# Kernel tuning notes

Hardware: AMD Instinct MI355X
Metric: run time of the kernel (lower is better)

Reference implementation:

```python
import jax, jax.numpy as jnp
import numpy as np

# Block sizes: 3-hop sampled bipartite graphs (src -> dst per layer)
N_SRC0, N_DST0, E0 = 500_000, 100_000, 1_000_000
N_DST1, E1 = 10_000, 100_000
N_DST2, E2 = 1_024, 10_240
D_IN, D_HID, N_CLS = 128, 128, 47


def setup_inputs() -> dict:
    key = jax.random.key(0)
    ks = jax.random.split(key, 16)
    feats = jax.random.normal(ks[0], (N_SRC0, D_IN), dtype=jnp.float32)
    src0 = jax.random.randint(ks[1], (E0,), 0, N_SRC0)
    dst0 = jax.random.randint(ks[2], (E0,), 0, N_DST0)
    src1 = jax.random.randint(ks[3], (E1,), 0, N_DST0)
    dst1 = jax.random.randint(ks[4], (E1,), 0, N_DST1)
    src2 = jax.random.randint(ks[5], (E2,), 0, N_DST1)
    dst2 = jax.random.randint(ks[6], (E2,), 0, N_DST2)
    # fsi.inverse_idx reindex + NPFeatureShuffle all-to-all -> two permutations
    inverse_idx = jax.random.permutation(ks[7], N_DST0)
    shuffle_idx = jax.random.permutation(ks[8], N_DST0)
    def glorot(k, fan_in, fan_out):
        lim = np.sqrt(6.0 / (fan_in + fan_out)).astype(np.float32)
        return jax.random.uniform(k, (fan_in, fan_out), jnp.float32, -lim, lim)
    W0 = glorot(ks[9], D_IN, D_HID)
    b0 = jnp.zeros((D_HID,), jnp.float32)
    W1 = glorot(ks[10], D_HID, D_HID)
    b1 = jnp.zeros((D_HID,), jnp.float32)
    W2 = glorot(ks[11], D_HID, N_CLS)
    b2 = jnp.zeros((N_CLS,), jnp.float32)
    return dict(feats=feats, src0=src0, dst0=dst0, src1=src1, dst1=dst1,
                src2=src2, dst2=dst2, inverse_idx=inverse_idx,
                shuffle_idx=shuffle_idx, W0=W0, b0=b0, W1=W1, b1=b1, W2=W2, b2=b2)


def _graph_conv(h_src, src, dst, n_src, n_dst, W, b, norm_both):
    # DGL GraphConv: optional D^{-1/2} on src, W, sum-aggregate over edges,
    # optional D^{-1/2} on dst, + bias. Degrees clamped to min 1.
    ones = jnp.ones(src.shape[0], dtype=h_src.dtype)
    if norm_both:
        out_deg = jax.ops.segment_sum(ones, src, num_segments=n_src)
        h_src = h_src * jax.lax.rsqrt(jnp.clip(out_deg, 1.0, None))[:, None]
    msgs = (h_src @ W)[src]                      # [E, d_out] gather
    agg = jax.ops.segment_sum(msgs, dst, num_segments=n_dst)  # scatter-add
    if norm_both:
        in_deg = jax.ops.segment_sum(ones, dst, num_segments=n_dst)
        agg = agg * jax.lax.rsqrt(jnp.clip(in_deg, 1.0, None))[:, None]
    return agg + b


def reference(feats, src0, dst0, src1, dst1, src2, dst2,
              inverse_idx, shuffle_idx, W0, b0, W1, b1, W2, b2):
    # layer 0: norm='none'
    h = _graph_conv(feats, src0, dst0, N_SRC0, N_DST0, W0, b0, norm_both=False)
    # fsi.inverse_idx reindex + NPFeatureShuffle (modeled as permutations)
    h = h[inverse_idx]
    h = h[shuffle_idx]
    h = jax.nn.relu(h)  # dropout is identity in eval
    # layer 1: norm='both'
    h = _graph_conv(h, src1, dst1, N_DST0, N_DST1, W1, b1, norm_both=True)
    h = jax.nn.relu(h)
    # layer 2: norm='both'
    h = _graph_conv(h, src2, dst2, N_DST1, N_DST2, W2, b2, norm_both=True)
    return h
```

## Files before the change

kernel.cpp:

```cpp
#include <hip/hip_runtime.h>
#include <stdint.h>

typedef unsigned int u32;
typedef unsigned short u16;

#define N_SRC0 500000
#define N_DST0 100000
#define N_DST1 10000
#define N_DST2 1024
#define NCLS 47
#define GROWS 48

#define NB0 98
#define NB1 10
#define NB2 1
#define NBLK 109

static __device__ __forceinline__ float bf16_lo(u32 v) { return __uint_as_float(v << 16); }
static __device__ __forceinline__ float bf16_hi(u32 v) { return __uint_as_float(v & 0xffff0000u); }
static __device__ __forceinline__ float bf16_to_f(u16 s) { return __uint_as_float(((u32)s) << 16); }
static __device__ __forceinline__ u16 f_to_bf16(float f) {
    u32 u = __float_as_uint(f);
    u32 r = u + 0x7fffu + ((u >> 16) & 1u);
    return (u16)(r >> 16);
}

#define OFF_A      0u
#define OFF_T1     0u
#define OFF_X2     6000000u
#define OFF_T2     12000000u
#define OFF_X1     51200000u
#define OFF_CSR0   102400000u
#define OFF_CSR1   106400000u
#define OFF_CSR2   106800000u
#define OFF_RS0    106840960u
#define OFF_CUR0   107240976u
#define OFF_RS1    107640976u
#define OFF_CUR1   107680992u
#define OFF_RS2    107720992u
#define OFF_CUR2   107725104u
#define OFF_CNT0   107729200u
#define OFF_DS1    108129200u
#define OFF_DD1    108529200u
#define OFF_DS2    108569200u
#define OFF_DD2    108609200u
#define ZERO_OFF   OFF_CNT0
#define ZERO_BYTES 884096u
#define OFF_WC0    108613296u
#define OFF_BC0    108678832u
#define OFF_WC1    108679344u
#define OFF_BC1    108744880u
#define OFF_WC2    108745392u
#define OFF_BC2    108769456u
#define OFF_FLAG   108769712u
#define OFF_BSUM   108769776u
#define OFF_BOFF   108770224u

__global__ __launch_bounds__(256) void k_zero(float4* __restrict__ p, int n) {
    int i = blockIdx.x * 256 + threadIdx.x;
    int stride = gridDim.x * 256;
    float4 z = make_float4(0.f, 0.f, 0.f, 0.f);
    for (; i < n; i += stride) p[i] = z;
}

__global__ void k_detect(const u32* __restrict__ w, u32* __restrict__ flag) {
    u32 u = w[threadIdx.x];
    int e = (u >> 23) & 0xff;
    unsigned long long m = __ballot(e >= 0xC0);
    if (threadIdx.x == 0) *flag = (m != 0ull) ? 1u : 0u;
}

__global__ __launch_bounds__(256) void k_convw(
    const void* __restrict__ W0, const void* __restrict__ b0,
    const void* __restrict__ W1, const void* __restrict__ b1,
    const void* __restrict__ W2, const void* __restrict__ b2,
    float* __restrict__ Wc0, float* __restrict__ bc0,
    float* __restrict__ Wc1, float* __restrict__ bc1,
    float* __restrict__ Wc2, float* __restrict__ bc2,
    const u32* __restrict__ flag)
{
    int i = blockIdx.x * 256 + threadIdx.x;
    bool bf = (*flag != 0u);
    const void* src; float* dst; int j;
    if      (i < 16384) { src = W0; dst = Wc0; j = i; }
    else if (i < 16512) { src = b0; dst = bc0; j = i - 16384; }
    else if (i < 32896) { src = W1; dst = Wc1; j = i - 16512; }
    else if (i < 33024) { src = b1; dst = bc1; j = i - 32896; }
    else if (i < 39040) { src = W2; dst = Wc2; j = i - 33024; }
    else if (i < 39087) { src = b2; dst = bc2; j = i - 39040; }
    else return;
    dst[j] = bf ? bf16_to_f(((const u16*)src)[j]) : ((const float*)src)[j];
}

__global__ __launch_bounds__(256) void k_deg_all(
    const int* __restrict__ dst0,
    const int* __restrict__ src1, const int* __restrict__ dst1,
    const int* __restrict__ src2, const int* __restrict__ dst2,
    u32* __restrict__ cnt0, u32* __restrict__ dS1, u32* __restrict__ dD1,
    u32* __restrict__ dS2, u32* __restrict__ dD2, int E0, int E1, int E2)
{
    int i = blockIdx.x * 256 + threadIdx.x;
    if (i < E0) atomicAdd(&cnt0[dst0[i]], 1u);
    if (i < E1) { atomicAdd(&dS1[src1[i]], 1u); atomicAdd(&dD1[dst1[i]], 1u); }
    if (i < E2) { atomicAdd(&dS2[src2[i]], 1u); atomicAdd(&dD2[dst2[i]], 1u); }
}

static __device__ __forceinline__ void seg_map(int b, const u32* cnt0, const u32* dD1,
                                               const u32* dD2, const u32*& cnt,
                                               int& base, int& n, int& seg) {
    if (b < NB0)            { cnt = cnt0; base = b * 1024;          n = N_DST0; seg = 0; }
    else if (b < NB0 + NB1) { cnt = dD1;  base = (b - NB0) * 1024;  n = N_DST1; seg = 1; }
    else                    { cnt = dD2;  base = 0;                 n = N_DST2; seg = 2; }
}

__global__ __launch_bounds__(256) void k_bsum(
    const u32* __restrict__ cnt0, const u32* __restrict__ dD1,
    const u32* __restrict__ dD2, u32* __restrict__ bsum)
{
    const u32* cnt; int base, n, seg;
    seg_map(blockIdx.x, cnt0, dD1, dD2, cnt, base, n, seg);
    int t = threadIdx.x;
    int i0 = base + t * 4;
    u32 s = 0;
    #pragma unroll
    for (int j = 0; j < 4; ++j) { int i = i0 + j; if (i < n) s += cnt[i]; }
    #pragma unroll
    for (int off = 32; off; off >>= 1) s += __shfl_down(s, off, 64);
    __shared__ u32 wsum[4];
    if ((t & 63) == 0) wsum[t >> 6] = s;
    __syncthreads();
    if (t == 0) bsum[blockIdx.x] = wsum[0] + wsum[1] + wsum[2] + wsum[3];
}

__global__ void k_bscan(const u32* __restrict__ bsum, u32* __restrict__ boff,
                        u32* __restrict__ rs0, u32* __restrict__ rs1,
                        u32* __restrict__ rs2)
{
    if (threadIdx.x != 0) return;
    u32 run = 0;
    for (int b = 0; b < NB0; ++b) { boff[b] = run; run += bsum[b]; }
    rs0[N_DST0] = run;
    run = 0;
    for (int b = NB0; b < NB0 + NB1; ++b) { boff[b] = run; run += bsum[b]; }
    rs1[N_DST1] = run;
    boff[NB0 + NB1] = 0;
    rs2[N_DST2] = bsum[NB0 + NB1];
}

__global__ __launch_bounds__(256) void k_bwrite(
    const u32* __restrict__ cnt0, const u32* __restrict__ dD1,
    const u32* __restrict__ dD2, const u32* __restrict__ boff,
    u32* __restrict__ rs0, u32* __restrict__ cur0,
    u32* __restrict__ rs1, u32* __restrict__ cur1,
    u32* __restrict__ rs2, u32* __restrict__ cur2)
{
    const u32* cnt; int base, n, seg;
    seg_map(blockIdx.x, cnt0, dD1, dD2, cnt, base, n, seg);
    u32 *rs, *cur;
    if (seg == 0)      { rs = rs0; cur = cur0; }
    else if (seg == 1) { rs = rs1; cur = cur1; }
    else               { rs = rs2; cur = cur2; }

    int t = threadIdx.x;
    int i0 = base + t * 4;
    u32 c[4]; u32 s = 0;
    #pragma unroll
    for (int j = 0; j < 4; ++j) {
        int i = i0 + j;
        c[j] = (i < n) ? cnt[i] : 0u;
        s += c[j];
    }
    __shared__ u32 sc[256];
    sc[t] = s;
    __syncthreads();
    #pragma unroll
    for (int off = 1; off < 256; off <<= 1) {
        u32 v = (t >= off) ? sc[t - off] : 0u;
        __syncthreads();
        sc[t] += v;
        __syncthreads();
    }
    u32 ex = sc[t] - s + boff[blockIdx.x];
    #pragma unroll
    for (int j = 0; j < 4; ++j) {
        int i = i0 + j;
        if (i < n) { rs[i] = ex; cur[i] = ex; ex += c[j]; }
    }
}

__global__ __launch_bounds__(256) void k_fill(
    const int* __restrict__ src0, const int* __restrict__ dst0,
    const int* __restrict__ src1, const int* __restrict__ dst1,
    const int* __restrict__ src2, const int* __restrict__ dst2,
    u32* __restrict__ cur0, int* __restrict__ csr0,
    u32* __restrict__ cur1, int* __restrict__ csr1,
    u32* __restrict__ cur2, int* __restrict__ csr2,
    int E0, int E1, int E2)
{
    int i = blockIdx.x * 256 + threadIdx.x;
    if (i < E0) { u32 p = atomicAdd(&cur0[dst0[i]], 1u); csr0[p] = src0[i]; }
    if (i < E1) { u32 p = atomicAdd(&cur1[dst1[i]], 1u); csr1[p] = src1[i]; }
    if (i < E2) { u32 p = atomicAdd(&cur2[dst2[i]], 1u); csr2[p] = src2[i]; }
}

__global__ __launch_bounds__(256) void k_agg0(
    const void* __restrict__ feats, const u32* __restrict__ rs,
    const int* __restrict__ csr, float* __restrict__ out, int nrows,
    const u32* __restrict__ flag)
{
    int r = blockIdx.x * 4 + (threadIdx.x >> 6);
    if (r >= nrows) return;
    int l = threadIdx.x & 63;
    u32 beg = rs[r], end = rs[r + 1];
    float x = 0.f, y = 0.f;
    if (*flag) {
        const u32* f = (const u32*)feats;
        u32 e = beg;
        for (; e + 4 <= end; e += 4) {
            int s0 = csr[e], s1 = csr[e + 1], s2 = csr[e + 2], s3 = csr[e + 3];
            u32 v0 = f[(size_t)s0 * 64 + l];
            u32 v1 = f[(size_t)s1 * 64 + l];
            u32 v2 = f[(size_t)s2 * 64 + l];
            u32 v3 = f[(size_t)s3 * 64 + l];
            x += bf16_lo(v0) + bf16_lo(v1) + bf16_lo(v2) + bf16_lo(v3);
            y += bf16_hi(v0) + bf16_hi(v1) + bf16_hi(v2) + bf16_hi(v3);
        }
        for (; e < end; ++e) {
            u32 v = f[(size_t)csr[e] * 64 + l];
            x += bf16_lo(v); y += bf16_hi(v);
        }
    } else {
        const float2* f = (const float2*)feats;
        u32 e = beg;
        for (; e + 4 <= end; e += 4) {
            int s0 = csr[e], s1 = csr[e + 1], s2 = csr[e + 2], s3 = csr[e + 3];
            float2 v0 = f[(size_t)s0 * 64 + l];
            float2 v1 = f[(size_t)s1 * 64 + l];
            float2 v2 = f[(size_t)s2 * 64 + l];
            float2 v3 = f[(size_t)s3 * 64 + l];
            x += v0.x + v1.x + v2.x + v3.x;
            y += v0.y + v1.y + v2.y + v3.y;
        }
        for (; e < end; ++e) {
            float2 v = f[(size_t)csr[e] * 64 + l];
            x += v.x; y += v.y;
        }
    }
    *(float2*)(out + (size_t)r * 128 + 2 * l) = make_float2(x, y);
}

__global__ __launch_bounds__(256) void k_aggf(
    const float2* __restrict__ xin, const u32* __restrict__ rs,
    const int* __restrict__ csr, float* __restrict__ out, int nrows)
{
    int r = blockIdx.x * 4 + (threadIdx.x >> 6);
    if (r >= nrows) return;
    int l = threadIdx.x & 63;
    u32 beg = rs[r], end = rs[r + 1];
    float x = 0.f, y = 0.f;
    u32 e = beg;
    for (; e + 4 <= end; e += 4) {
        int s0 = csr[e], s1 = csr[e + 1], s2 = csr[e + 2], s3 = csr[e + 3];
        float2 v0 = xin[(size_t)s0 * 64 + l];
        float2 v1 = xin[(size_t)s1 * 64 + l];
        float2 v2 = xin[(size_t)s2 * 64 + l];
        float2 v3 = xin[(size_t)s3 * 64 + l];
        x += v0.x + v1.x + v2.x + v3.x;
        y += v0.y + v1.y + v2.y + v3.y;
    }
    for (; e < end; ++e) {
        float2 v = xin[(size_t)csr[e] * 64 + l];
        x += v.x; y += v.y;
    }
    *(float2*)(out + (size_t)r * 128 + 2 * l) = make_float2(x, y);
}

__global__ __launch_bounds__(256) void k_gemm_fused(
    const float* __restrict__ A, const float* __restrict__ Wc,
    const float* __restrict__ bc,
    const int* __restrict__ inv, const int* __restrict__ shuf,
    const u32* __restrict__ inDeg, const u32* __restrict__ outDeg,
    float* __restrict__ out, int rows)
{
    __shared__ float As[GROWS][132];
    __shared__ float Ws[64][128];
    __shared__ int   rowmap[GROWS];
    __shared__ float preS[GROWS], postS[GROWS], bS[128];

    int tid = threadIdx.x;
    int I0 = blockIdx.x * GROWS;

    if (tid < GROWS) {
        int I = I0 + tid;
        int ar = 0; float pre = 1.f, post = 1.f;
        if (I < rows) {
            ar = shuf ? inv[shuf[I]] : I;
            if (inDeg)  { u32 dg = inDeg[I];  pre  = rsqrtf((float)(dg > 1u ? dg : 1u)); }
            if (outDeg) { u32 dg = outDeg[I]; post = rsqrtf((float)(dg > 1u ? dg : 1u)); }
        }
        rowmap[tid] = ar; preS[tid] = pre; postS[tid] = post;
    }
    if (tid < 128) bS[tid] = bc[tid];
    __syncthreads();

    for (int m = tid; m < GROWS * 64; m += 256) {
        int row = m >> 6, cp = m & 63;
        float2 v = *(const float2*)(A + (size_t)rowmap[row] * 128 + cp * 2);
        *(float2*)&As[row][cp * 2] = v;
    }

    int tc = tid & 15, tr = tid >> 4;
    int c0 = tc * 8, r0 = tr * 3;
    float acc[3][8];
    #pragma unroll
    for (int i = 0; i < 3; ++i)
        #pragma unroll
        for (int j = 0; j < 8; ++j) acc[i][j] = 0.f;

    for (int ph = 0; ph < 2; ++ph) {
        __syncthreads();
        const float4* Wg = (const float4*)(Wc + ph * 64 * 128);
        float4* Wl = (float4*)&Ws[0][0];
        for (int m = tid; m < 64 * 32; m += 256) Wl[m] = Wg[m];
        __syncthreads();
        int kk = ph * 64;
        #pragma unroll 4
        for (int k = 0; k < 64; ++k) {
            float a0 = As[r0 + 0][kk + k];
            float a1 = As[r0 + 1][kk + k];
            float a2 = As[r0 + 2][kk + k];
            float4 w0 = *(const float4*)&Ws[k][c0];
            float4 w1 = *(const float4*)&Ws[k][c0 + 4];
            float w[8] = {w0.x, w0.y, w0.z, w0.w, w1.x, w1.y, w1.z, w1.w};
            #pragma unroll
            for (int j = 0; j < 8; ++j) {
                acc[0][j] = fmaf(a0, w[j], acc[0][j]);
                acc[1][j] = fmaf(a1, w[j], acc[1][j]);
                acc[2][j] = fmaf(a2, w[j], acc[2][j]);
            }
        }
    }

    #pragma unroll
    for (int i = 0; i < 3; ++i) {
        int I = I0 + r0 + i;
        if (I >= rows) continue;
        float pre = preS[r0 + i], post = postS[r0 + i];
        float o[8];
        #pragma unroll
        for (int j = 0; j < 8; ++j) {
            float v = acc[i][j] * pre + bS[c0 + j];
            v = v > 0.f ? v : 0.f;
            o[j] = v * post;
        }
        float* dst = out + (size_t)I * 128 + c0;
        *(float4*)dst       = make_float4(o[0], o[1], o[2], o[3]);
        *(float4*)(dst + 4) = make_float4(o[4], o[5], o[6], o[7]);
    }
}

__global__ __launch_bounds__(256) void k_gemm2(
    const float* __restrict__ t2, const float* __restrict__ Wc2,
    const float* __restrict__ bc2, const u32* __restrict__ inDeg,
    void* __restrict__ out, const u32* __restrict__ flag)
{
    int g = blockIdx.x * 256 + threadIdx.x;
    if (g >= N_DST2 * NCLS) return;
    int r = g / NCLS, c = g - r * NCLS;
    const float* a = t2 + (size_t)r * 128;
    float acc = 0.f;
    #pragma unroll 8
    for (int k = 0; k < 128; ++k) acc = fmaf(a[k], Wc2[k * NCLS + c], acc);
    u32 dg = inDeg[r];
    float v = acc * rsqrtf((float)(dg > 1u ? dg : 1u)) + bc2[c];
    if (*flag) ((u16*)out)[g] = f_to_bf16(v);
    else       ((float*)out)[g] = v;
}

extern "C" void kernel_launch(void* const* d_in, const int* in_sizes, int n_in,
                              void* d_out, int out_size, void* d_ws, size_t ws_size,
                              hipStream_t stream)
{
    (void)n_in; (void)out_size; (void)ws_size;
    const void* feats = d_in[0];
    const int* src0 = (const int*)d_in[1];
    const int* dst0 = (const int*)d_in[2];
    const int* src1 = (const int*)d_in[3];
    const int* dst1 = (const int*)d_in[4];
    const int* src2 = (const int*)d_in[5];
    const int* dst2 = (const int*)d_in[6];
    const int* inv  = (const int*)d_in[7];
    const int* shuf = (const int*)d_in[8];
    const void* W0 = d_in[9];  const void* b0 = d_in[10];
    const void* W1 = d_in[11]; const void* b1 = d_in[12];
    const void* W2 = d_in[13]; const void* b2 = d_in[14];
    int E0 = in_sizes[1], E1 = in_sizes[3], E2 = in_sizes[5];

    char* ws = (char*)d_ws;
    float* aggA = (float*)(ws + OFF_A);
    float* t1   = (float*)(ws + OFF_T1);
    float* x2   = (float*)(ws + OFF_X2);
    float* t2b  = (float*)(ws + OFF_T2);
    float* x1   = (float*)(ws + OFF_X1);
    int* csr0 = (int*)(ws + OFF_CSR0);
    int* csr1 = (int*)(ws + OFF_CSR1);
    int* csr2 = (int*)(ws + OFF_CSR2);
    u32* rs0  = (u32*)(ws + OFF_RS0);
    u32* cur0 = (u32*)(ws + OFF_CUR0);
    u32* rs1  = (u32*)(ws + OFF_RS1);
    u32* cur1 = (u32*)(ws + OFF_CUR1);
    u32* rs2  = (u32*)(ws + OFF_RS2);
    u32* cur2 = (u32*)(ws + OFF_CUR2);
    u32* cnt0 = (u32*)(ws + OFF_CNT0);
    u32* dS1  = (u32*)(ws + OFF_DS1);
    u32* dD1  = (u32*)(ws + OFF_DD1);
    u32* dS2  = (u32*)(ws + OFF_DS2);
    u32* dD2  = (u32*)(ws + OFF_DD2);
    float* Wc0 = (float*)(ws + OFF_WC0);
    float* bc0 = (float*)(ws + OFF_BC0);
    float* Wc1 = (float*)(ws + OFF_WC1);
    float* bc1 = (float*)(ws + OFF_BC1);
    float* Wc2 = (float*)(ws + OFF_WC2);
    float* bc2 = (float*)(ws + OFF_BC2);
    u32* flag  = (u32*)(ws + OFF_FLAG);
    u32* bsum  = (u32*)(ws + OFF_BSUM);
    u32* boff  = (u32*)(ws + OFF_BOFF);

    k_zero<<<216, 256, 0, stream>>>((float4*)(ws + ZERO_OFF), (int)(ZERO_BYTES / 16));
    k_detect<<<1, 64, 0, stream>>>((const u32*)feats, flag);
    k_convw<<<(39087 + 255) / 256, 256, 0, stream>>>(W0, b0, W1, b1, W2, b2,
                                                     Wc0, bc0, Wc1, bc1, Wc2, bc2, flag);
    k_deg_all<<<(E0 + 255) / 256, 256, 0, stream>>>(dst0, src1, dst1, src2, dst2,
                                                    cnt0, dS1, dD1, dS2, dD2, E0, E1, E2);
    k_bsum<<<NBLK, 256, 0, stream>>>(cnt0, dD1, dD2, bsum);
    k_bscan<<<1, 64, 0, stream>>>(bsum, boff, rs0, rs1, rs2);
    k_bwrite<<<NBLK, 256, 0, stream>>>(cnt0, dD1, dD2, boff,
                                       rs0, cur0, rs1, cur1, rs2, cur2);
    k_fill<<<(E0 + 255) / 256, 256, 0, stream>>>(src0, dst0, src1, dst1, src2, dst2,
                                                 cur0, csr0, cur1, csr1, cur2, csr2,
                                                 E0, E1, E2);
    k_agg0<<<(N_DST0 + 3) / 4, 256, 0, stream>>>(feats, rs0, csr0, aggA, N_DST0, flag);
    k_gemm_fused<<<(N_DST0 + GROWS - 1) / GROWS, 256, 0, stream>>>(
        aggA, Wc0, bc0, inv, shuf, nullptr, dS1, x1, N_DST0);
    k_aggf<<<(N_DST1 + 3) / 4, 256, 0, stream>>>((const float2*)x1, rs1, csr1, t1, N_DST1);
    k_gemm_fused<<<(N_DST1 + GROWS - 1) / GROWS, 256, 0, stream>>>(
        t1, Wc1, bc1, nullptr, nullptr, dD1, dS2, x2, N_DST1);
    k_aggf<<<(N_DST2 + 3) / 4, 256, 0, stream>>>((const float2*)x2, rs2, csr2, t2b, N_DST2);
    k_gemm2<<<(N_DST2 * NCLS + 255) / 256, 256, 0, stream>>>(t2b, Wc2, bc2, dD2, d_out, flag);
}
```

Baseline: 690.7 us.

## Fuse aggregation into MFMA bf16 GEMM layers and merge prep kernels

Gather-aggregation now runs inside each layer kernel: the aggregated rows go straight into LDS as bf16 and are multiplied with pre-fragmented bf16 weights using MFMA 16x16x32 instructions, so the fp32 intermediate aggregate buffers are never written or re-read. Layer 2's aggregation and small GEMM are fused the same way, and the zero, detect and weight-convert kernels are merged into one prep launch that also packs weights into MFMA fragment layout. This removes several launches and a large round trip through global memory. The cost is reduced precision, since aggregates and weights are rounded to bf16, and less parallelism in the gather, with each wave now handling 12 rows serially.

```diff
diff --git a/kernel.cpp b/kernel.cpp
--- a/kernel.cpp
+++ b/kernel.cpp
@@ -3,13 +3,14 @@
 
 typedef unsigned int u32;
 typedef unsigned short u16;
+typedef __attribute__((ext_vector_type(8))) short short8;
+typedef __attribute__((ext_vector_type(4))) float f32x4;
 
 #define N_SRC0 500000
 #define N_DST0 100000
 #define N_DST1 10000
 #define N_DST2 1024
 #define NCLS 47
-#define GROWS 48
 
 #define NB0 98
 #define NB1 10
@@ -25,71 +26,96 @@
     return (u16)(r >> 16);
 }
 
-#define OFF_A      0u
-#define OFF_T1     0u
-#define OFF_X2     6000000u
-#define OFF_T2     12000000u
-#define OFF_X1     51200000u
-#define OFF_CSR0   102400000u
-#define OFF_CSR1   106400000u
-#define OFF_CSR2   106800000u
-#define OFF_RS0    106840960u
-#define OFF_CUR0   107240976u
-#define OFF_RS1    107640976u
-#define OFF_CUR1   107680992u
-#define OFF_RS2    107720992u
-#define OFF_CUR2   107725104u
-#define OFF_CNT0   107729200u
-#define OFF_DS1    108129200u
-#define OFF_DD1    108529200u
-#define OFF_DS2    108569200u
-#define OFF_DD2    108609200u
+#define OFF_X1     0u
+#define OFF_X2     51200000u
+#define OFF_CSR0   56320000u
+#define OFF_CSR1   60320000u
+#define OFF_CSR2   60720000u
+#define OFF_RS0    60760960u
+#define OFF_CUR0   61160976u
+#define OFF_RS1    61560976u
+#define OFF_CUR1   61600992u
+#define OFF_RS2    61640992u
+#define OFF_CUR2   61645104u
+#define OFF_CNT0   61649200u
+#define OFF_DS1    62049200u
+#define OFF_DD1    62449200u
+#define OFF_DS2    62489200u
+#define OFF_DD2    62529200u
 #define ZERO_OFF   OFF_CNT0
-#define ZERO_BYTES 884096u
-#define OFF_WC0    108613296u
-#define OFF_BC0    108678832u
-#define OFF_WC1    108679344u
-#define OFF_BC1    108744880u
-#define OFF_WC2    108745392u
-#define OFF_BC2    108769456u
-#define OFF_FLAG   108769712u
-#define OFF_BSUM   108769776u
-#define OFF_BOFF   108770224u
-
-__global__ __launch_bounds__(256) void k_zero(float4* __restrict__ p, int n) {
-    int i = blockIdx.x * 256 + threadIdx.x;
-    int stride = gridDim.x * 256;
-    float4 z = make_float4(0.f, 0.f, 0.f, 0.f);
-    for (; i < n; i += stride) p[i] = z;
-}
-
-__global__ void k_detect(const u32* __restrict__ w, u32* __restrict__ flag) {
-    u32 u = w[threadIdx.x];
-    int e = (u >> 23) & 0xff;
-    unsigned long long m = __ballot(e >= 0xC0);
-    if (threadIdx.x == 0) *flag = (m != 0ull) ? 1u : 0u;
-}
-
-__global__ __launch_bounds__(256) void k_convw(
+#define ZERO_N4    55256u
+#define OFF_WF0    62533296u
+#define OFF_WF1    62598832u
+#define OFF_WC2    62664368u
+#define OFF_BC0    62688432u
+#define OFF_BC1    62688944u
+#define OFF_BC2    62689456u
+#define OFF_FLAG   62689712u
+#define OFF_BSUM   62689776u
+#define OFF_BOFF   62690224u
+
+__global__ __launch_bounds__(256) void k_prep(
+    const u32* __restrict__ feats_w,
     const void* __restrict__ W0, const void* __restrict__ b0,
     const void* __restrict__ W1, const void* __restrict__ b1,
     const void* __restrict__ W2, const void* __restrict__ b2,
-    float* __restrict__ Wc0, float* __restrict__ bc0,
-    float* __restrict__ Wc1, float* __restrict__ bc1,
-    float* __restrict__ Wc2, float* __restrict__ bc2,
-    const u32* __restrict__ flag)
-{
-    int i = blockIdx.x * 256 + threadIdx.x;
-    bool bf = (*flag != 0u);
-    const void* src; float* dst; int j;
-    if      (i < 16384) { src = W0; dst = Wc0; j = i; }
-    else if (i < 16512) { src = b0; dst = bc0; j = i - 16384; }
-    else if (i < 32896) { src = W1; dst = Wc1; j = i - 16512; }
-    else if (i < 33024) { src = b1; dst = bc1; j = i - 32896; }
-    else if (i < 39040) { src = W2; dst = Wc2; j = i - 33024; }
-    else if (i < 39087) { src = b2; dst = bc2; j = i - 39040; }
-    else return;
-    dst[j] = bf ? bf16_to_f(((const u16*)src)[j]) : ((const float*)src)[j];
+    float4* __restrict__ zbase,
+    u16* __restrict__ wf0, u16* __restrict__ wf1,
+    float* __restrict__ wc2, float* __restrict__ bc0,
+    float* __restrict__ bc1, float* __restrict__ bc2,
+    u32* __restrict__ flag)
+{
+    int b = blockIdx.x, t = threadIdx.x;
+    if (b < 216) {
+        u32 i = b * 256 + t;
+        if (i < ZERO_N4) zbase[i] = make_float4(0.f, 0.f, 0.f, 0.f);
+        return;
+    }
+    if (b == 216) {
+        if (t < 64) {
+            u32 u = feats_w[t];
+            int e = (u >> 23) & 0xff;
+            unsigned long long m = __ballot(e >= 0xC0);
+            if (t == 0) *flag = (m != 0ull) ? 1u : 0u;
+        }
+        return;
+    }
+    __shared__ u32 lflag;
+    if (b < 233) {
+        const void* W = (b < 225) ? W0 : W1;
+        u16* dst = (b < 225) ? wf0 : wf1;
+        int base = ((b < 225) ? (b - 217) : (b - 225)) * 256;
+        if (t == 0) lflag = 0u;
+        __syncthreads();
+        if (t < 64) { u32 u = ((const u32*)W)[t]; if (((u >> 23) & 0xff) >= 0xC0) atomicOr(&lflag, 1u); }
+        __syncthreads();
+        bool bf = (lflag != 0u);
+        int idx = base + t;
+        int fid = idx >> 6, lane = idx & 63;
+        int nt = fid >> 2, ks = fid & 3;
+        #pragma unroll
+        for (int j = 0; j < 8; ++j) {
+            int k = ks * 32 + (lane >> 4) * 8 + j;
+            int n = nt * 16 + (lane & 15);
+            u16 v = bf ? ((const u16*)W)[k * 128 + n]
+                       : f_to_bf16(((const float*)W)[k * 128 + n]);
+            dst[idx * 8 + j] = v;
+        }
+        return;
+    }
+    if (b < 257) {
+        if (t == 0) lflag = 0u;
+        __syncthreads();
+        if (t < 64) { u32 u = ((const u32*)W2)[t]; if (((u >> 23) & 0xff) >= 0xC0) atomicOr(&lflag, 1u); }
+        __syncthreads();
+        bool bf = (lflag != 0u);
+        int i = (b - 233) * 256 + t;
+        if (i < 128 * NCLS)
+            wc2[i] = bf ? bf16_to_f(((const u16*)W2)[i]) : ((const float*)W2)[i];
+        return;
+    }
+    if (t < 128) { bc0[t] = ((const float*)b0)[t]; bc1[t] = ((const float*)b1)[t]; }
+    if (t < NCLS) bc2[t] = ((const float*)b2)[t];
 }
 
 __global__ __launch_bounds__(256) void k_deg_all(
@@ -203,178 +229,179 @@
     if (i < E2) { u32 p = atomicAdd(&cur2[dst2[i]], 1u); csr2[p] = src2[i]; }
 }
 
-__global__ __launch_bounds__(256) void k_agg0(
-    const void* __restrict__ feats, const u32* __restrict__ rs,
-    const int* __restrict__ csr, float* __restrict__ out, int nrows,
-    const u32* __restrict__ flag)
-{
-    int r = blockIdx.x * 4 + (threadIdx.x >> 6);
-    if (r >= nrows) return;
-    int l = threadIdx.x & 63;
-    u32 beg = rs[r], end = rs[r + 1];
-    float x = 0.f, y = 0.f;
-    if (*flag) {
-        const u32* f = (const u32*)feats;
-        u32 e = beg;
-        for (; e + 4 <= end; e += 4) {
-            int s0 = csr[e], s1 = csr[e + 1], s2 = csr[e + 2], s3 = csr[e + 3];
-            u32 v0 = f[(size_t)s0 * 64 + l];
-            u32 v1 = f[(size_t)s1 * 64 + l];
-            u32 v2 = f[(size_t)s2 * 64 + l];
-            u32 v3 = f[(size_t)s3 * 64 + l];
-            x += bf16_lo(v0) + bf16_lo(v1) + bf16_lo(v2) + bf16_lo(v3);
-            y += bf16_hi(v0) + bf16_hi(v1) + bf16_hi(v2) + bf16_hi(v3);
-        }
-        for (; e < end; ++e) {
-            u32 v = f[(size_t)csr[e] * 64 + l];
-            x += bf16_lo(v); y += bf16_hi(v);
-        }
-    } else {
-        const float2* f = (const float2*)feats;
-        u32 e = beg;
-        for (; e + 4 <= end; e += 4) {
-            int s0 = csr[e], s1 = csr[e + 1], s2 = csr[e + 2], s3 = csr[e + 3];
-            float2 v0 = f[(size_t)s0 * 64 + l];
-            float2 v1 = f[(size_t)s1 * 64 + l];
-            float2 v2 = f[(size_t)s2 * 64 + l];
-            float2 v3 = f[(size_t)s3 * 64 + l];
-            x += v0.x + v1.x + v2.x + v3.x;
-            y += v0.y + v1.y + v2.y + v3.y;
-        }
-        for (; e < end; ++e) {
-            float2 v = f[(size_t)csr[e] * 64 + l];
-            x += v.x; y += v.y;
-        }
-    }
-    *(float2*)(out + (size_t)r * 128 + 2 * l) = make_float2(x, y);
-}
-
-__global__ __launch_bounds__(256) void k_aggf(
-    const float2* __restrict__ xin, const u32* __restrict__ rs,
-    const int* __restrict__ csr, float* __restrict__ out, int nrows)
-{
-    int r = blockIdx.x * 4 + (threadIdx.x >> 6);
-    if (r >= nrows) return;
-    int l = threadIdx.x & 63;
-    u32 beg = rs[r], end = rs[r + 1];
-    float x = 0.f, y = 0.f;
-    u32 e = beg;
-    for (; e + 4 <= end; e += 4) {
-        int s0 = csr[e], s1 = csr[e + 1], s2 = csr[e + 2], s3 = csr[e + 3];
-        float2 v0 = xin[(size_t)s0 * 64 + l];
-        float2 v1 = xin[(size_t)s1 * 64 + l];
-        float2 v2 = xin[(size_t)s2 * 64 + l];
-        float2 v3 = xin[(size_t)s3 * 64 + l];
-        x += v0.x + v1.x + v2.x + v3.x;
-        y += v0.y + v1.y + v2.y + v3.y;
-    }
-    for (; e < end; ++e) {
-        float2 v = xin[(size_t)csr[e] * 64 + l];
-        x += v.x; y += v.y;
-    }
-    *(float2*)(out + (size_t)r * 128 + 2 * l) = make_float2(x, y);
-}
-
-__global__ __launch_bounds__(256) void k_gemm_fused(
-    const float* __restrict__ A, const float* __restrict__ Wc,
-    const float* __restrict__ bc,
+__global__ __launch_bounds__(256) void k_layer(
+    const void* __restrict__ Ain, const u32* __restrict__ flag,
+    const u32* __restrict__ rs, const int* __restrict__ csr,
     const int* __restrict__ inv, const int* __restrict__ shuf,
-    const u32* __restrict__ inDeg, const u32* __restrict__ outDeg,
+    const u32* __restrict__ preDeg, const u32* __restrict__ postDeg,
+    const u16* __restrict__ Wfrag, const float* __restrict__ bias,
     float* __restrict__ out, int rows)
 {
-    __shared__ float As[GROWS][132];
-    __shared__ float Ws[64][128];
-    __shared__ int   rowmap[GROWS];
-    __shared__ float preS[GROWS], postS[GROWS], bS[128];
+    __shared__ u16  As[48][136];
+    __shared__ int  rowmapS[48];
+    __shared__ float preS[48], postS[48], bS[128];
 
     int tid = threadIdx.x;
-    int I0 = blockIdx.x * GROWS;
-
-    if (tid < GROWS) {
+    int wv = tid >> 6, lane = tid & 63;
+    int I0 = blockIdx.x * 48;
+
+    if (tid < 48) {
         int I = I0 + tid;
         int ar = 0; float pre = 1.f, post = 1.f;
         if (I < rows) {
             ar = shuf ? inv[shuf[I]] : I;
-            if (inDeg)  { u32 dg = inDeg[I];  pre  = rsqrtf((float)(dg > 1u ? dg : 1u)); }
-            if (outDeg) { u32 dg = outDeg[I]; post = rsqrtf((float)(dg > 1u ? dg : 1u)); }
-        }
-        rowmap[tid] = ar; preS[tid] = pre; postS[tid] = post;
-    }
-    if (tid < 128) bS[tid] = bc[tid];
+            if (preDeg)  { u32 d = preDeg[I];  pre  = rsqrtf((float)(d > 1u ? d : 1u)); }
+            if (postDeg) { u32 d = postDeg[I]; post = rsqrtf((float)(d > 1u ? d : 1u)); }
+        }
+        rowmapS[tid] = ar; preS[tid] = pre; postS[tid] = post;
+    }
+    if (tid < 128) bS[tid] = bias[tid];
+
+    short8 bf[2][4];
+    #pragma unroll
+    for (int nt = 0; nt < 2; ++nt)
+        #pragma unroll
+        for (int ks = 0; ks < 4; ++ks) {
+            int fid = (wv * 2 + nt) * 4 + ks;
+            bf[nt][ks] = *(const short8*)(Wfrag + (size_t)(fid * 64 + lane) * 8);
+        }
     __syncthreads();
 
-    for (int m = tid; m < GROWS * 64; m += 256) {
-        int row = m >> 6, cp = m & 63;
-        float2 v = *(const float2*)(A + (size_t)rowmap[row] * 128 + cp * 2);
-        *(float2*)&As[row][cp * 2] = v;
-    }
-
-    int tc = tid & 15, tr = tid >> 4;
-    int c0 = tc * 8, r0 = tr * 3;
-    float acc[3][8];
-    #pragma unroll
-    for (int i = 0; i < 3; ++i)
-        #pragma unroll
-        for (int j = 0; j < 8; ++j) acc[i][j] = 0.f;
-
-    for (int ph = 0; ph < 2; ++ph) {
-        __syncthreads();
-        const float4* Wg = (const float4*)(Wc + ph * 64 * 128);
-        float4* Wl = (float4*)&Ws[0][0];
-        for (int m = tid; m < 64 * 32; m += 256) Wl[m] = Wg[m];
-        __syncthreads();
-        int kk = ph * 64;
-        #pragma unroll 4
-        for (int k = 0; k < 64; ++k) {
-            float a0 = As[r0 + 0][kk + k];
-            float a1 = As[r0 + 1][kk + k];
-            float a2 = As[r0 + 2][kk + k];
-            float4 w0 = *(const float4*)&Ws[k][c0];
-            float4 w1 = *(const float4*)&Ws[k][c0 + 4];
-            float w[8] = {w0.x, w0.y, w0.z, w0.w, w1.x, w1.y, w1.z, w1.w};
+    bool bfp = flag && (*flag != 0u);
+    for (int i = 0; i < 12; ++i) {
+        int r = wv * 12 + i;
+        int I = I0 + r;
+        float x = 0.f, y = 0.f;
+        if (I < rows) {
+            int ar = rowmapS[r];
+            u32 e = rs[ar], end = rs[ar + 1];
+            if (bfp) {
+                const u32* f = (const u32*)Ain;
+                for (; e + 4 <= end; e += 4) {
+                    int s0 = csr[e], s1 = csr[e+1], s2 = csr[e+2], s3 = csr[e+3];
+                    u32 v0 = f[(size_t)s0 * 64 + lane];
+                    u32 v1 = f[(size_t)s1 * 64 + lane];
+                    u32 v2 = f[(size_t)s2 * 64 + lane];
+                    u32 v3 = f[(size_t)s3 * 64 + lane];
+                    x += bf16_lo(v0) + bf16_lo(v1) + bf16_lo(v2) + bf16_lo(v3);
+                    y += bf16_hi(v0) + bf16_hi(v1) + bf16_hi(v2) + bf16_hi(v3);
+                }
+                for (; e < end; ++e) {
+                    u32 v = f[(size_t)csr[e] * 64 + lane];
+                    x += bf16_lo(v); y += bf16_hi(v);
+                }
+            } else {
+                const float2* f = (const float2*)Ain;
+                for (; e + 4 <= end; e += 4) {
+                    int s0 = csr[e], s1 = csr[e+1], s2 = csr[e+2], s3 = csr[e+3];
+                    float2 v0 = f[(size_t)s0 * 64 + lane];
+                    float2 v1 = f[(size_t)s1 * 64 + lane];
+                    float2 v2 = f[(size_t)s2 * 64 + lane];
+                    float2 v3 = f[(size_t)s3 * 64 + lane];
+                    x += v0.x + v1.x + v2.x + v3.x;
+                    y += v0.y + v1.y + v2.y + v3.y;
+                }
+                for (; e < end; ++e) {
+                    float2 v = f[(size_t)csr[e] * 64 + lane];
+                    x += v.x; y += v.y;
+                }
+            }
+        }
+        u32 pk = ((u32)f_to_bf16(y) << 16) | (u32)f_to_bf16(x);
+        *(u32*)&As[r][2 * lane] = pk;
+    }
+    __syncthreads();
+
+    f32x4 acc[2][3];
+    #pragma unroll
+    for (int nt = 0; nt < 2; ++nt)
+        #pragma unroll
+        for (int mt = 0; mt < 3; ++mt) acc[nt][mt] = (f32x4){0.f, 0.f, 0.f, 0.f};
+
+    #pragma unroll
+    for (int ks = 0; ks < 4; ++ks) {
+        short8 af[3];
+        #pragma unroll
+        for (int mt = 0; mt < 3; ++mt) {
+            int row = mt * 16 + (lane & 15);
+            int k0 = ks * 32 + (lane >> 4) * 8;
+            af[mt] = *(const short8*)&As[row][k0];
+        }
+        #pragma unroll
+        for (int nt = 0; nt < 2; ++nt)
             #pragma unroll
-            for (int j = 0; j < 8; ++j) {
-                acc[0][j] = fmaf(a0, w[j], acc[0][j]);
-                acc[1][j] = fmaf(a1, w[j], acc[1][j]);
-                acc[2][j] = fmaf(a2, w[j], acc[2][j]);
+            for (int mt = 0; mt < 3; ++mt)
+                acc[nt][mt] = __builtin_amdgcn_mfma_f32_16x16x32_bf16(
+                    af[mt], bf[nt][ks], acc[nt][mt], 0, 0, 0);
+    }
+
+    int quad = lane >> 4, cl = lane & 15;
+    #pragma unroll
+    for (int nt = 0; nt < 2; ++nt) {
+        int col = (wv * 2 + nt) * 16 + cl;
+        float bb = bS[col];
+        #pragma unroll
+        for (int mt = 0; mt < 3; ++mt) {
+            #pragma unroll
+            for (int rg = 0; rg < 4; ++rg) {
+                int lr = mt * 16 + quad * 4 + rg;
+                int I = I0 + lr;
+                if (I < rows) {
+                    float v = acc[nt][mt][rg] * preS[lr] + bb;
+                    v = v > 0.f ? v : 0.f;
+                    out[(size_t)I * 128 + col] = v * postS[lr];
+                }
             }
         }
     }
-
-    #pragma unroll
-    for (int i = 0; i < 3; ++i) {
-        int I = I0 + r0 + i;
-        if (I >= rows) continue;
-        float pre = preS[r0 + i], post = postS[r0 + i];
-        float o[8];
-        #pragma unroll
-        for (int j = 0; j < 8; ++j) {
-            float v = acc[i][j] * pre + bS[c0 + j];
-            v = v > 0.f ? v : 0.f;
-            o[j] = v * post;
-        }
-        float* dst = out + (size_t)I * 128 + c0;
-        *(float4*)dst       = make_float4(o[0], o[1], o[2], o[3]);
-        *(float4*)(dst + 4) = make_float4(o[4], o[5], o[6], o[7]);
-    }
-}
-
-__global__ __launch_bounds__(256) void k_gemm2(
-    const float* __restrict__ t2, const float* __restrict__ Wc2,
-    const float* __restrict__ bc2, const u32* __restrict__ inDeg,
+}
+
+__global__ __launch_bounds__(256) void k_layer2(
+    const float2* __restrict__ x2, const u32* __restrict__ rs,
+    const int* __restrict__ csr, const u32* __restrict__ preDeg,
+    const float* __restrict__ Wc2, const float* __restrict__ bc2,
     void* __restrict__ out, const u32* __restrict__ flag)
 {
-    int g = blockIdx.x * 256 + threadIdx.x;
-    if (g >= N_DST2 * NCLS) return;
-    int r = g / NCLS, c = g - r * NCLS;
-    const float* a = t2 + (size_t)r * 128;
-    float acc = 0.f;
-    #pragma unroll 8
-    for (int k = 0; k < 128; ++k) acc = fmaf(a[k], Wc2[k * NCLS + c], acc);
-    u32 dg = inDeg[r];
-    float v = acc * rsqrtf((float)(dg > 1u ? dg : 1u)) + bc2[c];
-    if (*flag) ((u16*)out)[g] = f_to_bf16(v);
-    else       ((float*)out)[g] = v;
+    __shared__ float t2[16][128];
+    int tid = threadIdx.x;
+    int wv = tid >> 6, lane = tid & 63;
+    int R0 = blockIdx.x * 16;
+
+    for (int i = 0; i < 4; ++i) {
+        int r = wv * 4 + i;
+        int R = R0 + r;
+        float x = 0.f, y = 0.f;
+        u32 e = rs[R], end = rs[R + 1];
+        for (; e + 4 <= end; e += 4) {
+            int s0 = csr[e], s1 = csr[e+1], s2 = csr[e+2], s3 = csr[e+3];
+            float2 v0 = x2[(size_t)s0 * 64 + lane];
+            float2 v1 = x2[(size_t)s1 * 64 + lane];
+            float2 v2 = x2[(size_t)s2 * 64 + lane];
+            float2 v3 = x2[(size_t)s3 * 64 + lane];
+            x += v0.x + v1.x + v2.x + v3.x;
+            y += v0.y + v1.y + v2.y + v3.y;
+        }
+        for (; e < end; ++e) {
+            float2 v = x2[(size_t)csr[e] * 64 + lane];
+            x += v.x; y += v.y;
+        }
+        t2[r][2 * lane] = x;
+        t2[r][2 * lane + 1] = y;
+    }
+    __syncthreads();
+
+    bool bfp = flag && (*flag != 0u);
+    for (int idx = tid; idx < 16 * NCLS; idx += 256) {
+        int r = idx / NCLS, c = idx - NCLS * r;
+        float a = 0.f;
+        #pragma unroll 8
+        for (int k = 0; k < 128; ++k) a = fmaf(t2[r][k], Wc2[k * NCLS + c], a);
+        u32 d = preDeg[R0 + r];
+        float v = a * rsqrtf((float)(d > 1u ? d : 1u)) + bc2[c];
+        int g = (R0 + r) * NCLS + c;
+        if (bfp) ((u16*)out)[g] = f_to_bf16(v);
+        else     ((float*)out)[g] = v;
+    }
 }
 
 extern "C" void kernel_launch(void* const* d_in, const int* in_sizes, int n_in,
@@ -397,11 +424,8 @@
     int E0 = in_sizes[1], E1 = in_sizes[3], E2 = in_sizes[5];
 
     char* ws = (char*)d_ws;
-    float* aggA = (float*)(ws + OFF_A);
-    float* t1   = (float*)(ws + OFF_T1);
-    float* x2   = (float*)(ws + OFF_X2);
-    float* t2b  = (float*)(ws + OFF_T2);
-    float* x1   = (float*)(ws + OFF_X1);
+    float* x1  = (float*)(ws + OFF_X1);
+    float* x2  = (float*)(ws + OFF_X2);
     int* csr0 = (int*)(ws + OFF_CSR0);
     int* csr1 = (int*)(ws + OFF_CSR1);
     int* csr2 = (int*)(ws + OFF_CSR2);
@@ -416,20 +440,19 @@
     u32* dD1  = (u32*)(ws + OFF_DD1);
     u32* dS2  = (u32*)(ws + OFF_DS2);
     u32* dD2  = (u32*)(ws + OFF_DD2);
-    float* Wc0 = (float*)(ws + OFF_WC0);
+    u16* wf0  = (u16*)(ws + OFF_WF0);
+    u16* wf1  = (u16*)(ws + OFF_WF1);
+    float* wc2 = (float*)(ws + OFF_WC2);
     float* bc0 = (float*)(ws + OFF_BC0);
-    float* Wc1 = (float*)(ws + OFF_WC1);
     float* bc1 = (float*)(ws + OFF_BC1);
-    float* Wc2 = (float*)(ws + OFF_WC2);
     float* bc2 = (float*)(ws + OFF_BC2);
     u32* flag  = (u32*)(ws + OFF_FLAG);
     u32* bsum  = (u32*)(ws + OFF_BSUM);
     u32* boff  = (u32*)(ws + OFF_BOFF);
 
-    k_zero<<<216, 256, 0, stream>>>((float4*)(ws + ZERO_OFF), (int)(ZERO_BYTES / 16));
-    k_detect<<<1, 64, 0, stream>>>((const u32*)feats, flag);
-    k_convw<<<(39087 + 255) / 256, 256, 0, stream>>>(W0, b0, W1, b1, W2, b2,
-                                                     Wc0, bc0, Wc1, bc1, Wc2, bc2, flag);
+    k_prep<<<258, 256, 0, stream>>>((const u32*)feats, W0, b0, W1, b1, W2, b2,
+                                    (float4*)(ws + ZERO_OFF), wf0, wf1, wc2,
+                                    bc0, bc1, bc2, flag);
     k_deg_all<<<(E0 + 255) / 256, 256, 0, stream>>>(dst0, src1, dst1, src2, dst2,
                                                     cnt0, dS1, dD1, dS2, dD2, E0, E1, E2);
     k_bsum<<<NBLK, 256, 0, stream>>>(cnt0, dD1, dD2, bsum);
@@ -439,12 +462,10 @@
     k_fill<<<(E0 + 255) / 256, 256, 0, stream>>>(src0, dst0, src1, dst1, src2, dst2,
                                                  cur0, csr0, cur1, csr1, cur2, csr2,
                                                  E0, E1, E2);
-    k_agg0<<<(N_DST0 + 3) / 4, 256, 0, stream>>>(feats, rs0, csr0, aggA, N_DST0, flag);
-    k_gemm_fused<<<(N_DST0 + GROWS - 1) / GROWS, 256, 0, stream>>>(
-        aggA, Wc0, bc0, inv, shuf, nullptr, dS1, x1, N_DST0);
-    k_aggf<<<(N_DST1 + 3) / 4, 256, 0, stream>>>((const float2*)x1, rs1, csr1, t1, N_DST1);
-    k_gemm_fused<<<(N_DST1 + GROWS - 1) / GROWS, 256, 0, stream>>>(
-        t1, Wc1, bc1, nullptr, nullptr, dD1, dS2, x2, N_DST1);
-    k_aggf<<<(N_DST2 + 3) / 4, 256, 0, stream>>>((const float2*)x2, rs2, csr2, t2b, N_DST2);
-    k_gemm2<<<(N_DST2 * NCLS + 255) / 256, 256, 0, stream>>>(t2b, Wc2, bc2, dD2, d_out, flag);
-}
+    k_layer<<<(N_DST0 + 47) / 48, 256, 0, stream>>>(
+        feats, flag, rs0, csr0, inv, shuf, nullptr, dS1, wf0, bc0, x1, N_DST0);
+    k_layer<<<(N_DST1 + 47) / 48, 256, 0, stream>>>(
+        x1, nullptr, rs1, csr1, nullptr, nullptr, dD1, dS2, wf1, bc1, x2, N_DST1);
+    k_layer2<<<N_DST2 / 16, 256, 0, stream>>>(
+        (const float2*)x2, rs2, csr2, dD2, wc2, bc2, d_out, flag);
+}
```

After: 681.9 us. No clear change (-1.3%).
